# Kernel tuning notes

Measured on AMD Instinct MI355X. Metric: run time of the kernel, lower is better.

## Reference

```python
import jax, jax.numpy as jnp
import numpy as np

N_NODES = 200000
N_BONDS = 220000
D = 128


def setup_inputs() -> dict:
    key = jax.random.key(0)
    ks = jax.random.split(key, 8)
    h = jax.random.normal(ks[0], (N_NODES, D), dtype=jnp.float32)
    src = jax.random.randint(ks[1], (N_BONDS,), 0, N_NODES, dtype=jnp.int64)
    dst = jax.random.randint(ks[2], (N_BONDS,), 0, N_NODES, dtype=jnp.int64)
    # MLP params (Sequential: Linear(256,128)+ReLU, Linear(128,128)+ReLU, Linear(128,2))
    W1 = jax.random.normal(ks[3], (2 * D, 128), dtype=jnp.float32) * (1.0 / np.sqrt(2 * D))
    b1 = jnp.zeros((128,), dtype=jnp.float32)
    W2 = jax.random.normal(ks[4], (128, 128), dtype=jnp.float32) * (1.0 / np.sqrt(128))
    b2 = jnp.zeros((128,), dtype=jnp.float32)
    W3 = jax.random.normal(ks[5], (128, 2), dtype=jnp.float32) * (1.0 / np.sqrt(128))
    b3 = jnp.zeros((2,), dtype=jnp.float32)
    return {"h": h, "src": src, "dst": dst,
            "W1": W1, "b1": b1, "W2": W2, "b2": b2, "W3": W3, "b3": b3}


def _mlp(x, W1, b1, W2, b2, W3, b3):
    x = jax.nn.relu(x @ W1 + b1)
    x = jax.nn.relu(x @ W2 + b2)
    return x @ W3 + b3


def reference(h, src, dst, W1, b1, W2, b2, W3, b3):
    # forward edges: (src -> dst); reverse edges: (dst -> src)
    h_src = h[src]            # [E, D] gather
    h_dst = h[dst]            # [E, D] gather
    h_forward = jnp.concatenate([h_src, h_dst], axis=1)  # [E, 2D]
    h_reverse = jnp.concatenate([h_dst, h_src], axis=1)  # [E, 2D]
    return (_mlp(h_forward, W1, b1, W2, b2, W3, b3)
            + _mlp(h_reverse, W1, b1, W2, b2, W3, b3))
```

## Files before the change

kernel.cpp:

```cpp
#include <hip/hip_runtime.h>
#include <hip/hip_bf16.h>
#include <stdint.h>


typedef __attribute__((ext_vector_type(8))) short bf16x8;
typedef __attribute__((ext_vector_type(4))) float f32x4;

__device__ __forceinline__ float bf2f(unsigned u16) {
    union { unsigned u; float f; } v; v.u = u16 << 16;
    return v.f;
}

__device__ __forceinline__ int swz(int f, int c) {
    return f * 128 + ((c ^ (f & 7)) << 3);
}

__device__ __forceinline__ bf16x8 addrelu8(uint4 a, uint4 b) {
    union { uint4 v; unsigned u[4]; } A, B;
    A.v = a; B.v = b;
    union { bf16x8 v; __hip_bfloat162 h[4]; } R;
#pragma unroll
    for (int i = 0; i < 4; ++i) {
        float a0 = bf2f(A.u[i] & 0xFFFFu), a1 = bf2f(A.u[i] >> 16);
        float b0 = bf2f(B.u[i] & 0xFFFFu), b1 = bf2f(B.u[i] >> 16);
        R.h[i] = __float22bfloat162_rn(float2{fmaxf(a0 + b0, 0.f),
                                              fmaxf(a1 + b1, 0.f)});
    }
    return R.v;
}

__device__ __forceinline__ uint4 pack8(const float* v) {
    union { uint4 u; __hip_bfloat162 h[4]; } R;
#pragma unroll
    for (int i = 0; i < 4; ++i)
        R.h[i] = __float22bfloat162_rn(float2{v[2 * i], v[2 * i + 1]});
    return R.u;
}

#define MFMA(a, b, c) __builtin_amdgcn_mfma_f32_16x16x32_bf16((a), (b), (c), 0, 0, 0)

__global__ __launch_bounds__(512, 2) void node_proj(
    const float* __restrict__ h, const float* __restrict__ W1,
    const float* __restrict__ b1, unsigned short* __restrict__ P, int nodes) {
    __shared__ unsigned short W1s[256 * 128];

    int t = threadIdx.x;
    int lane = t & 63;
    int wv = t >> 6;
    int ml = lane & 15, quad = lane >> 4;

    {
        int j = t >> 1, half = t & 1;
        const float* col = (j < 128) ? (W1 + j) : (W1 + 128 * 128 + (j - 128));
#pragma unroll
        for (int ci = 0; ci < 8; ++ci) {
            int c = half * 8 + ci;
            float v[8];
#pragma unroll
            for (int l = 0; l < 8; ++l)
                v[l] = col[(c * 8 + l) * 128];
            *(uint4*)(W1s + swz(j, c)) = pack8(v);
        }
    }

    int tile = blockIdx.x;
    int node = tile * 128 + wv * 16 + ml;
    int nodeL = (node < nodes) ? node : (nodes - 1);
    const float4* hp = (const float4*)(h + (size_t)nodeL * 128);
    float4 hreg[8];
#pragma unroll
    for (int kk = 0; kk < 4; ++kk) {
        hreg[2 * kk]     = hp[kk * 8 + quad * 2];
        hreg[2 * kk + 1] = hp[kk * 8 + quad * 2 + 1];
    }

    __syncthreads();

    bf16x8 bfrag[4];
#pragma unroll
    for (int kk = 0; kk < 4; ++kk) {
        union { bf16x8 v; __hip_bfloat162 hh[4]; } R;
        float4 x = hreg[2 * kk], y = hreg[2 * kk + 1];
        R.hh[0] = __float22bfloat162_rn(float2{x.x, x.y});
        R.hh[1] = __float22bfloat162_rn(float2{x.z, x.w});
        R.hh[2] = __float22bfloat162_rn(float2{y.x, y.y});
        R.hh[3] = __float22bfloat162_rn(float2{y.z, y.w});
        bfrag[kk] = R.v;
    }

    f32x4 acc[16] = {};
#pragma unroll
    for (int kk = 0; kk < 4; ++kk) {
#pragma unroll
        for (int ct = 0; ct < 16; ++ct) {
            bf16x8 afrag = *(const bf16x8*)(W1s + swz(ct * 16 + ml, kk * 4 + quad));
            acc[ct] = MFMA(afrag, bfrag[kk], acc[ct]);
        }
    }

    __syncthreads();

    unsigned* slice = (unsigned*)W1s + wv * 2048;
#pragma unroll
    for (int ct = 0; ct < 16; ++ct) {
        int fbase = ct * 16 + quad * 4;
        float v0 = acc[ct][0], v1 = acc[ct][1];
        float v2 = acc[ct][2], v3 = acc[ct][3];
        if (fbase >= 128) {
            float4 bv = *(const float4*)(b1 + (fbase - 128));
            v0 += bv.x; v1 += bv.y; v2 += bv.z; v3 += bv.w;
        }
        union { uint2 u; __hip_bfloat162 h2[2]; } o;
        o.h2[0] = __float22bfloat162_rn(float2{v0, v1});
        o.h2[1] = __float22bfloat162_rn(float2{v2, v3});
        int c = ct * 2 + (quad >> 1);
        int idx = ml * 128 + ((c ^ ml) << 2) + ((quad & 1) << 1);
        *(uint2*)(slice + idx) = o.u;
    }
#pragma unroll
    for (int i = 0; i < 8; ++i) {
        int n = i * 2 + (lane >> 5);
        int cr = lane & 31;
        uint4 val = *(const uint4*)(slice + n * 128 + ((cr ^ n) << 2));
        int gnode = tile * 128 + wv * 16 + n;
        if (gnode < nodes)
            *(uint4*)((unsigned*)(P + (size_t)gnode * 256) + cr * 4) = val;
    }
}

__global__ __launch_bounds__(512, 2) void edge_mlp(
    const unsigned short* __restrict__ P, const int* __restrict__ src,
    const int* __restrict__ dst, const float* __restrict__ W2,
    const float* __restrict__ b2, const float* __restrict__ W3,
    const float* __restrict__ b3, float* __restrict__ out, int E) {
    __shared__ unsigned short W2s[128 * 128];

    int t = threadIdx.x;
    int lane = t & 63;
    int wv = t >> 6;
    int ml = lane & 15, quad = lane >> 4;

    {
        int f = t >> 2, q4 = t & 3;
        const float* col = W2 + f;
#pragma unroll
        for (int ci = 0; ci < 4; ++ci) {
            int c = q4 * 4 + ci;
            float v[8];
#pragma unroll
            for (int l = 0; l < 8; ++l)
                v[l] = col[(c * 8 + l) * 128];
            *(uint4*)(W2s + swz(f, c)) = pack8(v);
        }
    }

    int e = blockIdx.x * 128 + wv * 16 + ml;
    int ec = (e < E) ? e : (E - 1);
    int si = src[ec], di = dst[ec];
    const unsigned short* Ps = P + (size_t)si * 256;
    const unsigned short* Pd = P + (size_t)di * 256;

    uint4 g[4][4];
#pragma unroll
    for (int kk = 0; kk < 4; ++kk) {
        int ko = kk * 32 + quad * 8;
        g[kk][0] = *(const uint4*)(Ps + ko);
        g[kk][1] = *(const uint4*)(Ps + 128 + ko);
        g[kk][2] = *(const uint4*)(Pd + ko);
        g[kk][3] = *(const uint4*)(Pd + 128 + ko);
    }

    __syncthreads();

    f32x4 acc[2][8] = {};
#pragma unroll
    for (int kk = 0; kk < 4; ++kk) {
        bf16x8 afw = addrelu8(g[kk][0], g[kk][3]);
        bf16x8 arv = addrelu8(g[kk][2], g[kk][1]);
#pragma unroll
        for (int ct = 0; ct < 8; ++ct) {
            bf16x8 bfrag = *(const bf16x8*)(W2s + swz(ct * 16 + ml, kk * 4 + quad));
            acc[0][ct] = MFMA(afw, bfrag, acc[0][ct]);
            acc[1][ct] = MFMA(arv, bfrag, acc[1][ct]);
        }
    }

    float w30[8], w31[8], b2v[8];
#pragma unroll
    for (int ct = 0; ct < 8; ++ct) {
        int c = ct * 16 + ml;
        w30[ct] = W3[c * 2 + 0];
        w31[ct] = W3[c * 2 + 1];
        b2v[ct] = b2[c];
    }
    float p0[2][4], p1[2][4];
#pragma unroll
    for (int rt = 0; rt < 2; ++rt)
#pragma unroll
        for (int reg = 0; reg < 4; ++reg) { p0[rt][reg] = 0.f; p1[rt][reg] = 0.f; }
#pragma unroll
    for (int rt = 0; rt < 2; ++rt)
#pragma unroll
        for (int ct = 0; ct < 8; ++ct)
#pragma unroll
            for (int reg = 0; reg < 4; ++reg) {
                float h2 = fmaxf(acc[rt][ct][reg] + b2v[ct], 0.f);
                p0[rt][reg] += h2 * w30[ct];
                p1[rt][reg] += h2 * w31[ct];
            }
#pragma unroll
    for (int m = 1; m < 16; m <<= 1) {
#pragma unroll
        for (int rt = 0; rt < 2; ++rt)
#pragma unroll
            for (int reg = 0; reg < 4; ++reg) {
                p0[rt][reg] += __shfl_xor(p0[rt][reg], m);
                p1[rt][reg] += __shfl_xor(p1[rt][reg], m);
            }
    }

    if (ml < 2) {
        float bb = 2.f * b3[ml];
#pragma unroll
        for (int reg = 0; reg < 4; ++reg) {
            int ee = blockIdx.x * 128 + wv * 16 + quad * 4 + reg;
            if (ee < E) {
                float v = (ml == 0) ? (p0[0][reg] + p0[1][reg])
                                    : (p1[0][reg] + p1[1][reg]);
                out[(size_t)ee * 2 + ml] = v + bb;
            }
        }
    }
}

extern "C" void kernel_launch(void* const* d_in, const int* in_sizes, int n_in,
                              void* d_out, int out_size, void* d_ws, size_t ws_size,
                              hipStream_t stream) {
    (void)n_in; (void)out_size; (void)ws_size;
    const float* h  = (const float*)d_in[0];
    const int*   sr = (const int*)d_in[1];
    const int*   ds = (const int*)d_in[2];
    const float* W1 = (const float*)d_in[3];
    const float* b1 = (const float*)d_in[4];
    const float* W2 = (const float*)d_in[5];
    const float* b2 = (const float*)d_in[6];
    const float* W3 = (const float*)d_in[7];
    const float* b3 = (const float*)d_in[8];
    float* out = (float*)d_out;

    int nodes = in_sizes[0] / 128;
    int E = in_sizes[1];

    unsigned short* P = (unsigned short*)d_ws;

    int ntiles = (nodes + 127) / 128;
    node_proj<<<ntiles, 512, 0, stream>>>(h, W1, b1, P, nodes);

    int etiles = (E + 127) / 128;
    edge_mlp<<<etiles, 512, 0, stream>>>(P, sr, ds, W2, b2, W3, b3, out, E);
}
```

Baseline: 247.1 us.

## Make node and edge kernels persistent with register prefetch of next tile

Both kernels now run a capped grid of at most 512 blocks, each looping over a contiguous range of tiles. The shared-memory weight staging is paid once per block instead of once per tile, and the next tile's inputs (h rows or gathered P rows plus indices) are prefetched into registers while the current tile's MFMAs run. The node kernel also drops the LDS transpose and writes P directly with 8-byte stores, and launch_bounds no longer request two blocks per CU. Risks are higher register pressure from the double-buffered gathers, less coalesced P writes, and load imbalance because ranges are split evenly regardless of tail.

```diff
diff --git a/kernel.cpp b/kernel.cpp
--- a/kernel.cpp
+++ b/kernel.cpp
@@ -39,9 +39,10 @@
 
 #define MFMA(a, b, c) __builtin_amdgcn_mfma_f32_16x16x32_bf16((a), (b), (c), 0, 0, 0)
 
-__global__ __launch_bounds__(512, 2) void node_proj(
+__global__ __launch_bounds__(512) void node_proj(
     const float* __restrict__ h, const float* __restrict__ W1,
-    const float* __restrict__ b1, unsigned short* __restrict__ P, int nodes) {
+    const float* __restrict__ b1, unsigned short* __restrict__ P,
+    int nodes, int ntiles, int per) {
     __shared__ unsigned short W1s[256 * 128];
 
     int t = threadIdx.x;
@@ -63,76 +64,85 @@
         }
     }
 
-    int tile = blockIdx.x;
-    int node = tile * 128 + wv * 16 + ml;
-    int nodeL = (node < nodes) ? node : (nodes - 1);
-    const float4* hp = (const float4*)(h + (size_t)nodeL * 128);
+    int t0 = blockIdx.x * per;
+    int t1 = t0 + per; if (t1 > ntiles) t1 = ntiles;
+
     float4 hreg[8];
-#pragma unroll
-    for (int kk = 0; kk < 4; ++kk) {
-        hreg[2 * kk]     = hp[kk * 8 + quad * 2];
-        hreg[2 * kk + 1] = hp[kk * 8 + quad * 2 + 1];
+    if (t0 < t1) {
+        int nd = t0 * 128 + wv * 16 + ml;
+        if (nd >= nodes) nd = nodes - 1;
+        const float4* hp = (const float4*)(h + (size_t)nd * 128);
+#pragma unroll
+        for (int kk = 0; kk < 4; ++kk) {
+            hreg[2 * kk]     = hp[kk * 8 + quad * 2];
+            hreg[2 * kk + 1] = hp[kk * 8 + quad * 2 + 1];
+        }
     }
 
     __syncthreads();
 
-    bf16x8 bfrag[4];
-#pragma unroll
-    for (int kk = 0; kk < 4; ++kk) {
-        union { bf16x8 v; __hip_bfloat162 hh[4]; } R;
-        float4 x = hreg[2 * kk], y = hreg[2 * kk + 1];
-        R.hh[0] = __float22bfloat162_rn(float2{x.x, x.y});
-        R.hh[1] = __float22bfloat162_rn(float2{x.z, x.w});
-        R.hh[2] = __float22bfloat162_rn(float2{y.x, y.y});
-        R.hh[3] = __float22bfloat162_rn(float2{y.z, y.w});
-        bfrag[kk] = R.v;
-    }
-
-    f32x4 acc[16] = {};
-#pragma unroll
-    for (int kk = 0; kk < 4; ++kk) {
-#pragma unroll
-        for (int ct = 0; ct < 16; ++ct) {
-            bf16x8 afrag = *(const bf16x8*)(W1s + swz(ct * 16 + ml, kk * 4 + quad));
-            acc[ct] = MFMA(afrag, bfrag[kk], acc[ct]);
-        }
-    }
-
-    __syncthreads();
-
-    unsigned* slice = (unsigned*)W1s + wv * 2048;
-#pragma unroll
-    for (int ct = 0; ct < 16; ++ct) {
-        int fbase = ct * 16 + quad * 4;
-        float v0 = acc[ct][0], v1 = acc[ct][1];
-        float v2 = acc[ct][2], v3 = acc[ct][3];
-        if (fbase >= 128) {
-            float4 bv = *(const float4*)(b1 + (fbase - 128));
-            v0 += bv.x; v1 += bv.y; v2 += bv.z; v3 += bv.w;
-        }
-        union { uint2 u; __hip_bfloat162 h2[2]; } o;
-        o.h2[0] = __float22bfloat162_rn(float2{v0, v1});
-        o.h2[1] = __float22bfloat162_rn(float2{v2, v3});
-        int c = ct * 2 + (quad >> 1);
-        int idx = ml * 128 + ((c ^ ml) << 2) + ((quad & 1) << 1);
-        *(uint2*)(slice + idx) = o.u;
-    }
-#pragma unroll
-    for (int i = 0; i < 8; ++i) {
-        int n = i * 2 + (lane >> 5);
-        int cr = lane & 31;
-        uint4 val = *(const uint4*)(slice + n * 128 + ((cr ^ n) << 2));
-        int gnode = tile * 128 + wv * 16 + n;
-        if (gnode < nodes)
-            *(uint4*)((unsigned*)(P + (size_t)gnode * 256) + cr * 4) = val;
-    }
-}
-
-__global__ __launch_bounds__(512, 2) void edge_mlp(
+    for (int tile = t0; tile < t1; ++tile) {
+        bf16x8 bfrag[4];
+#pragma unroll
+        for (int kk = 0; kk < 4; ++kk) {
+            union { bf16x8 v; __hip_bfloat162 hh[4]; } R;
+            float4 x = hreg[2 * kk], y = hreg[2 * kk + 1];
+            R.hh[0] = __float22bfloat162_rn(float2{x.x, x.y});
+            R.hh[1] = __float22bfloat162_rn(float2{x.z, x.w});
+            R.hh[2] = __float22bfloat162_rn(float2{y.x, y.y});
+            R.hh[3] = __float22bfloat162_rn(float2{y.z, y.w});
+            bfrag[kk] = R.v;
+        }
+
+        int node = tile * 128 + wv * 16 + ml;
+
+        if (tile + 1 < t1) {
+            int nd = (tile + 1) * 128 + wv * 16 + ml;
+            if (nd >= nodes) nd = nodes - 1;
+            const float4* hp = (const float4*)(h + (size_t)nd * 128);
+#pragma unroll
+            for (int kk = 0; kk < 4; ++kk) {
+                hreg[2 * kk]     = hp[kk * 8 + quad * 2];
+                hreg[2 * kk + 1] = hp[kk * 8 + quad * 2 + 1];
+            }
+        }
+
+        f32x4 acc[16] = {};
+#pragma unroll
+        for (int kk = 0; kk < 4; ++kk) {
+#pragma unroll
+            for (int ct = 0; ct < 16; ++ct) {
+                bf16x8 afrag = *(const bf16x8*)(W1s + swz(ct * 16 + ml, kk * 4 + quad));
+                acc[ct] = MFMA(afrag, bfrag[kk], acc[ct]);
+            }
+        }
+
+        if (node < nodes) {
+            unsigned short* prow = P + (size_t)node * 256;
+#pragma unroll
+            for (int ct = 0; ct < 16; ++ct) {
+                int fbase = ct * 16 + quad * 4;
+                float v0 = acc[ct][0], v1 = acc[ct][1];
+                float v2 = acc[ct][2], v3 = acc[ct][3];
+                if (fbase >= 128) {
+                    float4 bv = *(const float4*)(b1 + (fbase - 128));
+                    v0 += bv.x; v1 += bv.y; v2 += bv.z; v3 += bv.w;
+                }
+                union { uint2 u; __hip_bfloat162 h2[2]; } o;
+                o.h2[0] = __float22bfloat162_rn(float2{v0, v1});
+                o.h2[1] = __float22bfloat162_rn(float2{v2, v3});
+                *(uint2*)(prow + fbase) = o.u;
+            }
+        }
+    }
+}
+
+__global__ __launch_bounds__(512) void edge_mlp(
     const unsigned short* __restrict__ P, const int* __restrict__ src,
     const int* __restrict__ dst, const float* __restrict__ W2,
     const float* __restrict__ b2, const float* __restrict__ W3,
-    const float* __restrict__ b3, float* __restrict__ out, int E) {
+    const float* __restrict__ b3, float* __restrict__ out,
+    int E, int etiles, int per) {
     __shared__ unsigned short W2s[128 * 128];
 
     int t = threadIdx.x;
@@ -151,37 +161,6 @@
             for (int l = 0; l < 8; ++l)
                 v[l] = col[(c * 8 + l) * 128];
             *(uint4*)(W2s + swz(f, c)) = pack8(v);
-        }
-    }
-
-    int e = blockIdx.x * 128 + wv * 16 + ml;
-    int ec = (e < E) ? e : (E - 1);
-    int si = src[ec], di = dst[ec];
-    const unsigned short* Ps = P + (size_t)si * 256;
-    const unsigned short* Pd = P + (size_t)di * 256;
-
-    uint4 g[4][4];
-#pragma unroll
-    for (int kk = 0; kk < 4; ++kk) {
-        int ko = kk * 32 + quad * 8;
-        g[kk][0] = *(const uint4*)(Ps + ko);
-        g[kk][1] = *(const uint4*)(Ps + 128 + ko);
-        g[kk][2] = *(const uint4*)(Pd + ko);
-        g[kk][3] = *(const uint4*)(Pd + 128 + ko);
-    }
-
-    __syncthreads();
-
-    f32x4 acc[2][8] = {};
-#pragma unroll
-    for (int kk = 0; kk < 4; ++kk) {
-        bf16x8 afw = addrelu8(g[kk][0], g[kk][3]);
-        bf16x8 arv = addrelu8(g[kk][2], g[kk][1]);
-#pragma unroll
-        for (int ct = 0; ct < 8; ++ct) {
-            bf16x8 bfrag = *(const bf16x8*)(W2s + swz(ct * 16 + ml, kk * 4 + quad));
-            acc[0][ct] = MFMA(afw, bfrag, acc[0][ct]);
-            acc[1][ct] = MFMA(arv, bfrag, acc[1][ct]);
         }
     }
 
@@ -193,41 +172,110 @@
         w31[ct] = W3[c * 2 + 1];
         b2v[ct] = b2[c];
     }
-    float p0[2][4], p1[2][4];
-#pragma unroll
-    for (int rt = 0; rt < 2; ++rt)
-#pragma unroll
-        for (int reg = 0; reg < 4; ++reg) { p0[rt][reg] = 0.f; p1[rt][reg] = 0.f; }
-#pragma unroll
-    for (int rt = 0; rt < 2; ++rt)
-#pragma unroll
-        for (int ct = 0; ct < 8; ++ct)
+    float bb0 = 2.f * b3[0], bb1 = 2.f * b3[1];
+
+    int t0 = blockIdx.x * per;
+    int t1 = t0 + per; if (t1 > etiles) t1 = etiles;
+
+    int si2 = 0, di2 = 0;
+    uint4 g[4][4];
+    if (t0 < t1) {
+        int e0 = t0 * 128 + wv * 16 + ml;
+        int ec = (e0 < E) ? e0 : (E - 1);
+        int si = src[ec], di = dst[ec];
+        const unsigned short* Ps = P + (size_t)si * 256;
+        const unsigned short* Pd = P + (size_t)di * 256;
+#pragma unroll
+        for (int kk = 0; kk < 4; ++kk) {
+            int ko = kk * 32 + quad * 8;
+            g[kk][0] = *(const uint4*)(Ps + ko);
+            g[kk][1] = *(const uint4*)(Ps + 128 + ko);
+            g[kk][2] = *(const uint4*)(Pd + ko);
+            g[kk][3] = *(const uint4*)(Pd + 128 + ko);
+        }
+        if (t0 + 1 < t1) {
+            int e2 = (t0 + 1) * 128 + wv * 16 + ml;
+            int ec2 = (e2 < E) ? e2 : (E - 1);
+            si2 = src[ec2]; di2 = dst[ec2];
+        }
+    }
+
+    __syncthreads();
+
+    for (int tile = t0; tile < t1; ++tile) {
+        bf16x8 afw[4], arv[4];
+#pragma unroll
+        for (int kk = 0; kk < 4; ++kk) {
+            afw[kk] = addrelu8(g[kk][0], g[kk][3]);
+            arv[kk] = addrelu8(g[kk][2], g[kk][1]);
+        }
+
+        int ebase = tile * 128 + wv * 16;
+
+        if (tile + 1 < t1) {
+            const unsigned short* Ps = P + (size_t)si2 * 256;
+            const unsigned short* Pd = P + (size_t)di2 * 256;
+#pragma unroll
+            for (int kk = 0; kk < 4; ++kk) {
+                int ko = kk * 32 + quad * 8;
+                g[kk][0] = *(const uint4*)(Ps + ko);
+                g[kk][1] = *(const uint4*)(Ps + 128 + ko);
+                g[kk][2] = *(const uint4*)(Pd + ko);
+                g[kk][3] = *(const uint4*)(Pd + 128 + ko);
+            }
+            if (tile + 2 < t1) {
+                int e2 = (tile + 2) * 128 + wv * 16 + ml;
+                int ec2 = (e2 < E) ? e2 : (E - 1);
+                si2 = src[ec2]; di2 = dst[ec2];
+            }
+        }
+
+        f32x4 acc[2][8] = {};
+#pragma unroll
+        for (int kk = 0; kk < 4; ++kk) {
+#pragma unroll
+            for (int ct = 0; ct < 8; ++ct) {
+                bf16x8 bfrag = *(const bf16x8*)(W2s + swz(ct * 16 + ml, kk * 4 + quad));
+                acc[0][ct] = MFMA(afw[kk], bfrag, acc[0][ct]);
+                acc[1][ct] = MFMA(arv[kk], bfrag, acc[1][ct]);
+            }
+        }
+
+        float p0[2][4], p1[2][4];
+#pragma unroll
+        for (int rt = 0; rt < 2; ++rt)
+#pragma unroll
+            for (int reg = 0; reg < 4; ++reg) { p0[rt][reg] = 0.f; p1[rt][reg] = 0.f; }
+#pragma unroll
+        for (int rt = 0; rt < 2; ++rt)
+#pragma unroll
+            for (int ct = 0; ct < 8; ++ct)
+#pragma unroll
+                for (int reg = 0; reg < 4; ++reg) {
+                    float h2 = fmaxf(acc[rt][ct][reg] + b2v[ct], 0.f);
+                    p0[rt][reg] += h2 * w30[ct];
+                    p1[rt][reg] += h2 * w31[ct];
+                }
+#pragma unroll
+        for (int m = 1; m < 16; m <<= 1) {
+#pragma unroll
+            for (int rt = 0; rt < 2; ++rt)
+#pragma unroll
+                for (int reg = 0; reg < 4; ++reg) {
+                    p0[rt][reg] += __shfl_xor(p0[rt][reg], m);
+                    p1[rt][reg] += __shfl_xor(p1[rt][reg], m);
+                }
+        }
+
+        if (ml < 2) {
 #pragma unroll
             for (int reg = 0; reg < 4; ++reg) {
-                float h2 = fmaxf(acc[rt][ct][reg] + b2v[ct], 0.f);
-                p0[rt][reg] += h2 * w30[ct];
-                p1[rt][reg] += h2 * w31[ct];
-            }
-#pragma unroll
-    for (int m = 1; m < 16; m <<= 1) {
-#pragma unroll
-        for (int rt = 0; rt < 2; ++rt)
-#pragma unroll
-            for (int reg = 0; reg < 4; ++reg) {
-                p0[rt][reg] += __shfl_xor(p0[rt][reg], m);
-                p1[rt][reg] += __shfl_xor(p1[rt][reg], m);
-            }
-    }
-
-    if (ml < 2) {
-        float bb = 2.f * b3[ml];
-#pragma unroll
-        for (int reg = 0; reg < 4; ++reg) {
-            int ee = blockIdx.x * 128 + wv * 16 + quad * 4 + reg;
-            if (ee < E) {
-                float v = (ml == 0) ? (p0[0][reg] + p0[1][reg])
-                                    : (p1[0][reg] + p1[1][reg]);
-                out[(size_t)ee * 2 + ml] = v + bb;
+                int ee = ebase + quad * 4 + reg;
+                if (ee < E) {
+                    float v = (ml == 0) ? (p0[0][reg] + p0[1][reg] + bb0)
+                                        : (p1[0][reg] + p1[1][reg] + bb1);
+                    out[(size_t)ee * 2 + ml] = v;
+                }
             }
         }
     }
@@ -254,8 +302,12 @@
     unsigned short* P = (unsigned short*)d_ws;
 
     int ntiles = (nodes + 127) / 128;
-    node_proj<<<ntiles, 512, 0, stream>>>(h, W1, b1, P, nodes);
+    int ngrid = (ntiles < 512) ? ntiles : 512;
+    int nper = (ntiles + ngrid - 1) / ngrid;
+    node_proj<<<ngrid, 512, 0, stream>>>(h, W1, b1, P, nodes, ntiles, nper);
 
     int etiles = (E + 127) / 128;
-    edge_mlp<<<etiles, 512, 0, stream>>>(P, sr, ds, W2, b2, W3, b3, out, E);
-}
+    int egrid = (etiles < 512) ? etiles : 512;
+    int eper = (etiles + egrid - 1) / egrid;
+    edge_mlp<<<egrid, 512, 0, stream>>>(P, sr, ds, W2, b2, W3, b3, out, E, etiles, eper);
+}
```

Result: slower. 469.5 us (+90.0%).

## Persistent node projection with pre-transposed bf16 W1 and prefetched node rows

Applied to the files above, without the earlier changes.

Adds a small kernel that transposes and converts W1 to bf16 once, so each node_proj block copies it straight into LDS instead of doing strided fp32 loads. node_proj becomes persistent (capped at 512 blocks), loops over several 128-node tiles and prefetches the next tile's h rows into registers while the MFMAs run. The LDS-staged coalesced output write is replaced by direct 8-byte stores per lane, and launch bounds ask for 4 blocks per CU. The aim is to cut the repeated weight-staging cost and hide h load latency, at the cost of less coalesced P stores and an extra kernel launch.

```diff
diff --git a/kernel.cpp b/kernel.cpp
--- a/kernel.cpp
+++ b/kernel.cpp
@@ -9,6 +9,12 @@
 __device__ __forceinline__ float bf2f(unsigned u16) {
     union { unsigned u; float f; } v; v.u = u16 << 16;
     return v.f;
+}
+__device__ __forceinline__ unsigned short f2bf(float f) {
+    union { float f; unsigned u; } v; v.f = f;
+    unsigned u = v.u;
+    unsigned r = u + 0x7FFFu + ((u >> 16) & 1u);
+    return (unsigned short)(r >> 16);
 }
 
 __device__ __forceinline__ int swz(int f, int c) {
@@ -39,9 +45,20 @@
 
 #define MFMA(a, b, c) __builtin_amdgcn_mfma_f32_16x16x32_bf16((a), (b), (c), 0, 0, 0)
 
-__global__ __launch_bounds__(512, 2) void node_proj(
-    const float* __restrict__ h, const float* __restrict__ W1,
-    const float* __restrict__ b1, unsigned short* __restrict__ P, int nodes) {
+__global__ void prep_weights(const float* __restrict__ W1,
+                             unsigned short* __restrict__ W1t) {
+    int idx = blockIdx.x * 256 + threadIdx.x;
+    if (idx < 256 * 128) {
+        int j = idx >> 7, k = idx & 127;
+        float v = (j < 128) ? W1[k * 128 + j] : W1[(k + 128) * 128 + (j - 128)];
+        W1t[idx] = f2bf(v);
+    }
+}
+
+__global__ __launch_bounds__(512, 4) void node_proj(
+    const float* __restrict__ h, const unsigned short* __restrict__ W1t,
+    const float* __restrict__ b1, unsigned short* __restrict__ P,
+    int nodes, int ntiles, int per) {
     __shared__ unsigned short W1s[256 * 128];
 
     int t = threadIdx.x;
@@ -50,81 +67,83 @@
     int ml = lane & 15, quad = lane >> 4;
 
     {
-        int j = t >> 1, half = t & 1;
-        const float* col = (j < 128) ? (W1 + j) : (W1 + 128 * 128 + (j - 128));
-#pragma unroll
-        for (int ci = 0; ci < 8; ++ci) {
-            int c = half * 8 + ci;
-            float v[8];
-#pragma unroll
-            for (int l = 0; l < 8; ++l)
-                v[l] = col[(c * 8 + l) * 128];
-            *(uint4*)(W1s + swz(j, c)) = pack8(v);
-        }
-    }
-
-    int tile = blockIdx.x;
-    int node = tile * 128 + wv * 16 + ml;
-    int nodeL = (node < nodes) ? node : (nodes - 1);
-    const float4* hp = (const float4*)(h + (size_t)nodeL * 128);
+        int r = t >> 1, half = t & 1;
+        const uint4* src = (const uint4*)(W1t + (size_t)r * 128 + half * 64);
+#pragma unroll
+        for (int i = 0; i < 8; ++i)
+            *(uint4*)(W1s + swz(r, half * 8 + i)) = src[i];
+    }
+
+    int t0 = blockIdx.x * per;
+    int t1 = t0 + per; if (t1 > ntiles) t1 = ntiles;
+
     float4 hreg[8];
-#pragma unroll
-    for (int kk = 0; kk < 4; ++kk) {
-        hreg[2 * kk]     = hp[kk * 8 + quad * 2];
-        hreg[2 * kk + 1] = hp[kk * 8 + quad * 2 + 1];
+    if (t0 < t1) {
+        int nd = t0 * 128 + wv * 16 + ml;
+        if (nd >= nodes) nd = nodes - 1;
+        const float4* hp = (const float4*)(h + (size_t)nd * 128);
+#pragma unroll
+        for (int kk = 0; kk < 4; ++kk) {
+            hreg[2 * kk]     = hp[kk * 8 + quad * 2];
+            hreg[2 * kk + 1] = hp[kk * 8 + quad * 2 + 1];
+        }
     }
 
     __syncthreads();
 
-    bf16x8 bfrag[4];
-#pragma unroll
-    for (int kk = 0; kk < 4; ++kk) {
-        union { bf16x8 v; __hip_bfloat162 hh[4]; } R;
-        float4 x = hreg[2 * kk], y = hreg[2 * kk + 1];
-        R.hh[0] = __float22bfloat162_rn(float2{x.x, x.y});
-        R.hh[1] = __float22bfloat162_rn(float2{x.z, x.w});
-        R.hh[2] = __float22bfloat162_rn(float2{y.x, y.y});
-        R.hh[3] = __float22bfloat162_rn(float2{y.z, y.w});
-        bfrag[kk] = R.v;
-    }
-
-    f32x4 acc[16] = {};
-#pragma unroll
-    for (int kk = 0; kk < 4; ++kk) {
-#pragma unroll
-        for (int ct = 0; ct < 16; ++ct) {
-            bf16x8 afrag = *(const bf16x8*)(W1s + swz(ct * 16 + ml, kk * 4 + quad));
-            acc[ct] = MFMA(afrag, bfrag[kk], acc[ct]);
-        }
-    }
-
-    __syncthreads();
-
-    unsigned* slice = (unsigned*)W1s + wv * 2048;
-#pragma unroll
-    for (int ct = 0; ct < 16; ++ct) {
-        int fbase = ct * 16 + quad * 4;
-        float v0 = acc[ct][0], v1 = acc[ct][1];
-        float v2 = acc[ct][2], v3 = acc[ct][3];
-        if (fbase >= 128) {
-            float4 bv = *(const float4*)(b1 + (fbase - 128));
-            v0 += bv.x; v1 += bv.y; v2 += bv.z; v3 += bv.w;
-        }
-        union { uint2 u; __hip_bfloat162 h2[2]; } o;
-        o.h2[0] = __float22bfloat162_rn(float2{v0, v1});
-        o.h2[1] = __float22bfloat162_rn(float2{v2, v3});
-        int c = ct * 2 + (quad >> 1);
-        int idx = ml * 128 + ((c ^ ml) << 2) + ((quad & 1) << 1);
-        *(uint2*)(slice + idx) = o.u;
-    }
-#pragma unroll
-    for (int i = 0; i < 8; ++i) {
-        int n = i * 2 + (lane >> 5);
-        int cr = lane & 31;
-        uint4 val = *(const uint4*)(slice + n * 128 + ((cr ^ n) << 2));
-        int gnode = tile * 128 + wv * 16 + n;
-        if (gnode < nodes)
-            *(uint4*)((unsigned*)(P + (size_t)gnode * 256) + cr * 4) = val;
+    for (int tile = t0; tile < t1; ++tile) {
+        bf16x8 bfrag[4];
+#pragma unroll
+        for (int kk = 0; kk < 4; ++kk) {
+            union { bf16x8 v; __hip_bfloat162 hh[4]; } R;
+            float4 x = hreg[2 * kk], y = hreg[2 * kk + 1];
+            R.hh[0] = __float22bfloat162_rn(float2{x.x, x.y});
+            R.hh[1] = __float22bfloat162_rn(float2{x.z, x.w});
+            R.hh[2] = __float22bfloat162_rn(float2{y.x, y.y});
+            R.hh[3] = __float22bfloat162_rn(float2{y.z, y.w});
+            bfrag[kk] = R.v;
+        }
+
+        int node = tile * 128 + wv * 16 + ml;
+
+        if (tile + 1 < t1) {
+            int nd = (tile + 1) * 128 + wv * 16 + ml;
+            if (nd >= nodes) nd = nodes - 1;
+            const float4* hp = (const float4*)(h + (size_t)nd * 128);
+#pragma unroll
+            for (int kk = 0; kk < 4; ++kk) {
+                hreg[2 * kk]     = hp[kk * 8 + quad * 2];
+                hreg[2 * kk + 1] = hp[kk * 8 + quad * 2 + 1];
+            }
+        }
+
+        f32x4 acc[16] = {};
+#pragma unroll
+        for (int kk = 0; kk < 4; ++kk) {
+#pragma unroll
+            for (int ct = 0; ct < 16; ++ct) {
+                bf16x8 afrag = *(const bf16x8*)(W1s + swz(ct * 16 + ml, kk * 4 + quad));
+                acc[ct] = MFMA(afrag, bfrag[kk], acc[ct]);
+            }
+        }
+
+        if (node < nodes) {
+            unsigned short* prow = P + (size_t)node * 256;
+#pragma unroll
+            for (int ct = 0; ct < 16; ++ct) {
+                int fbase = ct * 16 + quad * 4;
+                float v0 = acc[ct][0], v1 = acc[ct][1];
+                float v2 = acc[ct][2], v3 = acc[ct][3];
+                if (fbase >= 128) {
+                    float4 bv = *(const float4*)(b1 + (fbase - 128));
+                    v0 += bv.x; v1 += bv.y; v2 += bv.z; v3 += bv.w;
+                }
+                union { uint2 u; __hip_bfloat162 h2[2]; } o;
+                o.h2[0] = __float22bfloat162_rn(float2{v0, v1});
+                o.h2[1] = __float22bfloat162_rn(float2{v2, v3});
+                *(uint2*)(prow + fbase) = o.u;
+            }
+        }
     }
 }
 
@@ -251,10 +270,15 @@
     int nodes = in_sizes[0] / 128;
     int E = in_sizes[1];
 
-    unsigned short* P = (unsigned short*)d_ws;
+    unsigned short* W1t = (unsigned short*)d_ws;
+    unsigned short* P   = W1t + 256 * 128;
+
+    prep_weights<<<128, 256, 0, stream>>>(W1, W1t);
 
     int ntiles = (nodes + 127) / 128;
-    node_proj<<<ntiles, 512, 0, stream>>>(h, W1, b1, P, nodes);
+    int ngrid = (ntiles < 512) ? ntiles : 512;
+    int nper = (ntiles + ngrid - 1) / ngrid;
+    node_proj<<<ngrid, 512, 0, stream>>>(h, W1t, b1, P, nodes, ntiles, nper);
 
     int etiles = (E + 127) / 128;
     edge_mlp<<<etiles, 512, 0, stream>>>(P, sr, ds, W2, b2, W3, b3, out, E);
```

Result: slower. 486.5 us (+96.9%).

## Fuse node projection and edge MLP into one persistent cooperative kernel

Applied to the files above, without the earlier changes.

Merges the two kernels into one persistent cooperative kernel. Each block first loops over node tiles to compute the projection, then passes a grid-wide sync, then loops over edge tiles. The goal is to load and convert W1/W2 into shared memory once per block instead of once per tile, and to remove the second kernel launch. In exchange it adds a grid sync and drops the LDS-staged coalesced write of P, so P is now written with scattered 8-byte stores. Loads are also no longer issued ahead of the first barrier, which reduces memory-latency overlap per tile.

```diff
diff --git a/kernel.cpp b/kernel.cpp
--- a/kernel.cpp
+++ b/kernel.cpp
@@ -1,6 +1,9 @@
 #include <hip/hip_runtime.h>
 #include <hip/hip_bf16.h>
+#include <hip/hip_cooperative_groups.h>
 #include <stdint.h>
+
+namespace cg = cooperative_groups;
 
 
 typedef __attribute__((ext_vector_type(8))) short bf16x8;
@@ -39,10 +42,15 @@
 
 #define MFMA(a, b, c) __builtin_amdgcn_mfma_f32_16x16x32_bf16((a), (b), (c), 0, 0, 0)
 
-__global__ __launch_bounds__(512, 2) void node_proj(
-    const float* __restrict__ h, const float* __restrict__ W1,
-    const float* __restrict__ b1, unsigned short* __restrict__ P, int nodes) {
-    __shared__ unsigned short W1s[256 * 128];
+__global__ __launch_bounds__(512, 2) void bond_fused(
+    const float* __restrict__ h, const int* __restrict__ src,
+    const int* __restrict__ dst, const float* __restrict__ W1,
+    const float* __restrict__ b1, const float* __restrict__ W2,
+    const float* __restrict__ b2, const float* __restrict__ W3,
+    const float* __restrict__ b3, unsigned short* __restrict__ P,
+    float* __restrict__ out, int nodes, int E, int ntiles, int etiles,
+    int nper, int eper) {
+    __shared__ unsigned short Ws[256 * 128];
 
     int t = threadIdx.x;
     int lane = t & 63;
@@ -50,95 +58,71 @@
     int ml = lane & 15, quad = lane >> 4;
 
     {
-        int j = t >> 1, half = t & 1;
+        int j = t >> 1, halfc = t & 1;
         const float* col = (j < 128) ? (W1 + j) : (W1 + 128 * 128 + (j - 128));
 #pragma unroll
         for (int ci = 0; ci < 8; ++ci) {
-            int c = half * 8 + ci;
+            int c = halfc * 8 + ci;
             float v[8];
 #pragma unroll
             for (int l = 0; l < 8; ++l)
                 v[l] = col[(c * 8 + l) * 128];
-            *(uint4*)(W1s + swz(j, c)) = pack8(v);
-        }
-    }
-
-    int tile = blockIdx.x;
-    int node = tile * 128 + wv * 16 + ml;
-    int nodeL = (node < nodes) ? node : (nodes - 1);
-    const float4* hp = (const float4*)(h + (size_t)nodeL * 128);
-    float4 hreg[8];
-#pragma unroll
-    for (int kk = 0; kk < 4; ++kk) {
-        hreg[2 * kk]     = hp[kk * 8 + quad * 2];
-        hreg[2 * kk + 1] = hp[kk * 8 + quad * 2 + 1];
-    }
-
+            *(uint4*)(Ws + swz(j, c)) = pack8(v);
+        }
+    }
     __syncthreads();
 
-    bf16x8 bfrag[4];
-#pragma unroll
-    for (int kk = 0; kk < 4; ++kk) {
-        union { bf16x8 v; __hip_bfloat162 hh[4]; } R;
-        float4 x = hreg[2 * kk], y = hreg[2 * kk + 1];
-        R.hh[0] = __float22bfloat162_rn(float2{x.x, x.y});
-        R.hh[1] = __float22bfloat162_rn(float2{x.z, x.w});
-        R.hh[2] = __float22bfloat162_rn(float2{y.x, y.y});
-        R.hh[3] = __float22bfloat162_rn(float2{y.z, y.w});
-        bfrag[kk] = R.v;
-    }
-
-    f32x4 acc[16] = {};
-#pragma unroll
-    for (int kk = 0; kk < 4; ++kk) {
-#pragma unroll
-        for (int ct = 0; ct < 16; ++ct) {
-            bf16x8 afrag = *(const bf16x8*)(W1s + swz(ct * 16 + ml, kk * 4 + quad));
-            acc[ct] = MFMA(afrag, bfrag[kk], acc[ct]);
+    {
+        int t0 = blockIdx.x * nper;
+        int t1 = t0 + nper; if (t1 > ntiles) t1 = ntiles;
+        for (int tile = t0; tile < t1; ++tile) {
+            int node = tile * 128 + wv * 16 + ml;
+            int nodeL = (node < nodes) ? node : (nodes - 1);
+            const float4* hp = (const float4*)(h + (size_t)nodeL * 128);
+            bf16x8 bfrag[4];
+#pragma unroll
+            for (int kk = 0; kk < 4; ++kk) {
+                float4 x = hp[kk * 8 + quad * 2];
+                float4 y = hp[kk * 8 + quad * 2 + 1];
+                union { bf16x8 v; __hip_bfloat162 hh[4]; } R;
+                R.hh[0] = __float22bfloat162_rn(float2{x.x, x.y});
+                R.hh[1] = __float22bfloat162_rn(float2{x.z, x.w});
+                R.hh[2] = __float22bfloat162_rn(float2{y.x, y.y});
+                R.hh[3] = __float22bfloat162_rn(float2{y.z, y.w});
+                bfrag[kk] = R.v;
+            }
+
+            f32x4 acc[16] = {};
+#pragma unroll
+            for (int kk = 0; kk < 4; ++kk) {
+#pragma unroll
+                for (int ct = 0; ct < 16; ++ct) {
+                    bf16x8 afrag = *(const bf16x8*)(Ws + swz(ct * 16 + ml, kk * 4 + quad));
+                    acc[ct] = MFMA(afrag, bfrag[kk], acc[ct]);
+                }
+            }
+
+            if (node < nodes) {
+                unsigned short* prow = P + (size_t)node * 256;
+#pragma unroll
+                for (int ct = 0; ct < 16; ++ct) {
+                    int fbase = ct * 16 + quad * 4;
+                    float v0 = acc[ct][0], v1 = acc[ct][1];
+                    float v2 = acc[ct][2], v3 = acc[ct][3];
+                    if (fbase >= 128) {
+                        float4 bv = *(const float4*)(b1 + (fbase - 128));
+                        v0 += bv.x; v1 += bv.y; v2 += bv.z; v3 += bv.w;
+                    }
+                    union { uint2 u; __hip_bfloat162 h2[2]; } o;
+                    o.h2[0] = __float22bfloat162_rn(float2{v0, v1});
+                    o.h2[1] = __float22bfloat162_rn(float2{v2, v3});
+                    *(uint2*)(prow + fbase) = o.u;
+                }
+            }
         }
     }
 
     __syncthreads();
-
-    unsigned* slice = (unsigned*)W1s + wv * 2048;
-#pragma unroll
-    for (int ct = 0; ct < 16; ++ct) {
-        int fbase = ct * 16 + quad * 4;
-        float v0 = acc[ct][0], v1 = acc[ct][1];
-        float v2 = acc[ct][2], v3 = acc[ct][3];
-        if (fbase >= 128) {
-            float4 bv = *(const float4*)(b1 + (fbase - 128));
-            v0 += bv.x; v1 += bv.y; v2 += bv.z; v3 += bv.w;
-        }
-        union { uint2 u; __hip_bfloat162 h2[2]; } o;
-        o.h2[0] = __float22bfloat162_rn(float2{v0, v1});
-        o.h2[1] = __float22bfloat162_rn(float2{v2, v3});
-        int c = ct * 2 + (quad >> 1);
-        int idx = ml * 128 + ((c ^ ml) << 2) + ((quad & 1) << 1);
-        *(uint2*)(slice + idx) = o.u;
-    }
-#pragma unroll
-    for (int i = 0; i < 8; ++i) {
-        int n = i * 2 + (lane >> 5);
-        int cr = lane & 31;
-        uint4 val = *(const uint4*)(slice + n * 128 + ((cr ^ n) << 2));
-        int gnode = tile * 128 + wv * 16 + n;
-        if (gnode < nodes)
-            *(uint4*)((unsigned*)(P + (size_t)gnode * 256) + cr * 4) = val;
-    }
-}
-
-__global__ __launch_bounds__(512, 2) void edge_mlp(
-    const unsigned short* __restrict__ P, const int* __restrict__ src,
-    const int* __restrict__ dst, const float* __restrict__ W2,
-    const float* __restrict__ b2, const float* __restrict__ W3,
-    const float* __restrict__ b3, float* __restrict__ out, int E) {
-    __shared__ unsigned short W2s[128 * 128];
-
-    int t = threadIdx.x;
-    int lane = t & 63;
-    int wv = t >> 6;
-    int ml = lane & 15, quad = lane >> 4;
 
     {
         int f = t >> 2, q4 = t & 3;
@@ -150,38 +134,7 @@
 #pragma unroll
             for (int l = 0; l < 8; ++l)
                 v[l] = col[(c * 8 + l) * 128];
-            *(uint4*)(W2s + swz(f, c)) = pack8(v);
-        }
-    }
-
-    int e = blockIdx.x * 128 + wv * 16 + ml;
-    int ec = (e < E) ? e : (E - 1);
-    int si = src[ec], di = dst[ec];
-    const unsigned short* Ps = P + (size_t)si * 256;
-    const unsigned short* Pd = P + (size_t)di * 256;
-
-    uint4 g[4][4];
-#pragma unroll
-    for (int kk = 0; kk < 4; ++kk) {
-        int ko = kk * 32 + quad * 8;
-        g[kk][0] = *(const uint4*)(Ps + ko);
-        g[kk][1] = *(const uint4*)(Ps + 128 + ko);
-        g[kk][2] = *(const uint4*)(Pd + ko);
-        g[kk][3] = *(const uint4*)(Pd + 128 + ko);
-    }
-
-    __syncthreads();
-
-    f32x4 acc[2][8] = {};
-#pragma unroll
-    for (int kk = 0; kk < 4; ++kk) {
-        bf16x8 afw = addrelu8(g[kk][0], g[kk][3]);
-        bf16x8 arv = addrelu8(g[kk][2], g[kk][1]);
-#pragma unroll
-        for (int ct = 0; ct < 8; ++ct) {
-            bf16x8 bfrag = *(const bf16x8*)(W2s + swz(ct * 16 + ml, kk * 4 + quad));
-            acc[0][ct] = MFMA(afw, bfrag, acc[0][ct]);
-            acc[1][ct] = MFMA(arv, bfrag, acc[1][ct]);
+            *(uint4*)(Ws + swz(f, c)) = pack8(v);
         }
     }
 
@@ -193,41 +146,74 @@
         w31[ct] = W3[c * 2 + 1];
         b2v[ct] = b2[c];
     }
-    float p0[2][4], p1[2][4];
-#pragma unroll
-    for (int rt = 0; rt < 2; ++rt)
-#pragma unroll
-        for (int reg = 0; reg < 4; ++reg) { p0[rt][reg] = 0.f; p1[rt][reg] = 0.f; }
-#pragma unroll
-    for (int rt = 0; rt < 2; ++rt)
-#pragma unroll
-        for (int ct = 0; ct < 8; ++ct)
-#pragma unroll
-            for (int reg = 0; reg < 4; ++reg) {
-                float h2 = fmaxf(acc[rt][ct][reg] + b2v[ct], 0.f);
-                p0[rt][reg] += h2 * w30[ct];
-                p1[rt][reg] += h2 * w31[ct];
-            }
-#pragma unroll
-    for (int m = 1; m < 16; m <<= 1) {
-#pragma unroll
-        for (int rt = 0; rt < 2; ++rt)
-#pragma unroll
-            for (int reg = 0; reg < 4; ++reg) {
-                p0[rt][reg] += __shfl_xor(p0[rt][reg], m);
-                p1[rt][reg] += __shfl_xor(p1[rt][reg], m);
-            }
-    }
-
-    if (ml < 2) {
-        float bb = 2.f * b3[ml];
-#pragma unroll
-        for (int reg = 0; reg < 4; ++reg) {
-            int ee = blockIdx.x * 128 + wv * 16 + quad * 4 + reg;
-            if (ee < E) {
-                float v = (ml == 0) ? (p0[0][reg] + p0[1][reg])
-                                    : (p1[0][reg] + p1[1][reg]);
-                out[(size_t)ee * 2 + ml] = v + bb;
+    float bb0 = 2.f * b3[0], bb1 = 2.f * b3[1];
+
+    cg::this_grid().sync();
+
+    {
+        int t0 = blockIdx.x * eper;
+        int t1 = t0 + eper; if (t1 > etiles) t1 = etiles;
+        for (int tile = t0; tile < t1; ++tile) {
+            int e = tile * 128 + wv * 16 + ml;
+            int ec = (e < E) ? e : (E - 1);
+            int si = src[ec], di = dst[ec];
+            const unsigned short* Ps = P + (size_t)si * 256;
+            const unsigned short* Pd = P + (size_t)di * 256;
+
+            f32x4 acc[2][8] = {};
+#pragma unroll
+            for (int kk = 0; kk < 4; ++kk) {
+                int ko = kk * 32 + quad * 8;
+                uint4 g0 = *(const uint4*)(Ps + ko);
+                uint4 g1 = *(const uint4*)(Ps + 128 + ko);
+                uint4 g2 = *(const uint4*)(Pd + ko);
+                uint4 g3 = *(const uint4*)(Pd + 128 + ko);
+                bf16x8 afw = addrelu8(g0, g3);
+                bf16x8 arv = addrelu8(g2, g1);
+#pragma unroll
+                for (int ct = 0; ct < 8; ++ct) {
+                    bf16x8 bfrag = *(const bf16x8*)(Ws + swz(ct * 16 + ml, kk * 4 + quad));
+                    acc[0][ct] = MFMA(afw, bfrag, acc[0][ct]);
+                    acc[1][ct] = MFMA(arv, bfrag, acc[1][ct]);
+                }
+            }
+
+            float p0[2][4], p1[2][4];
+#pragma unroll
+            for (int rt = 0; rt < 2; ++rt)
+#pragma unroll
+                for (int reg = 0; reg < 4; ++reg) { p0[rt][reg] = 0.f; p1[rt][reg] = 0.f; }
+#pragma unroll
+            for (int rt = 0; rt < 2; ++rt)
+#pragma unroll
+                for (int ct = 0; ct < 8; ++ct)
+#pragma unroll
+                    for (int reg = 0; reg < 4; ++reg) {
+                        float h2 = fmaxf(acc[rt][ct][reg] + b2v[ct], 0.f);
+                        p0[rt][reg] += h2 * w30[ct];
+                        p1[rt][reg] += h2 * w31[ct];
+                    }
+#pragma unroll
+            for (int m = 1; m < 16; m <<= 1) {
+#pragma unroll
+                for (int rt = 0; rt < 2; ++rt)
+#pragma unroll
+                    for (int reg = 0; reg < 4; ++reg) {
+                        p0[rt][reg] += __shfl_xor(p0[rt][reg], m);
+                        p1[rt][reg] += __shfl_xor(p1[rt][reg], m);
+                    }
+            }
+
+            if (ml < 2) {
+#pragma unroll
+                for (int reg = 0; reg < 4; ++reg) {
+                    int ee = tile * 128 + wv * 16 + quad * 4 + reg;
+                    if (ee < E) {
+                        float v = (ml == 0) ? (p0[0][reg] + p0[1][reg] + bb0)
+                                            : (p1[0][reg] + p1[1][reg] + bb1);
+                        out[(size_t)ee * 2 + ml] = v;
+                    }
+                }
             }
         }
     }
@@ -254,8 +240,22 @@
     unsigned short* P = (unsigned short*)d_ws;
 
     int ntiles = (nodes + 127) / 128;
-    node_proj<<<ntiles, 512, 0, stream>>>(h, W1, b1, P, nodes);
-
     int etiles = (E + 127) / 128;
-    edge_mlp<<<etiles, 512, 0, stream>>>(P, sr, ds, W2, b2, W3, b3, out, E);
-}
+
+    int maxb = 1;
+    hipOccupancyMaxActiveBlocksPerMultiprocessor(&maxb, (const void*)bond_fused, 512, 0);
+    if (maxb < 1) maxb = 1;
+    long long grid = 256LL * maxb;
+    if (grid > 512) grid = 512;
+    int gridi = (int)grid;
+
+    int nper = (ntiles + gridi - 1) / gridi;
+    int eper = (etiles + gridi - 1) / gridi;
+
+    void* args[] = {(void*)&h, (void*)&sr, (void*)&ds, (void*)&W1, (void*)&b1,
+                    (void*)&W2, (void*)&b2, (void*)&W3, (void*)&b3, (void*)&P,
+                    (void*)&out, (void*)&nodes, (void*)&E, (void*)&ntiles,
+                    (void*)&etiles, (void*)&nper, (void*)&eper};
+    hipLaunchCooperativeKernel((const void*)bond_fused, dim3(gridi), dim3(512),
+                               args, 0, stream);
+}
```

Result: slower. 410.6 us (+66.2%).
